# Optimization experiments

Hardware: AMD Instinct MI355X
Metric: run time of the kernel (lower is better)

Reference implementation:

```python
import jax, jax.numpy as jnp
import numpy as np

E, D, H, T = 64, 512, 1024, 256  # num_experts, dim, hidden_dim, tokens


def setup_inputs() -> dict:
    key = jax.random.key(0)
    k1, k2, k3, k4 = jax.random.split(key, 4)
    x = jax.random.normal(k1, (T, D), dtype=jnp.float32)
    expert_idx = jax.random.randint(k2, (T,), 0, E, dtype=jnp.int64)
    # kaiming_uniform-ish init scale for the batched expert weights
    fc1_w = jax.random.normal(k3, (E, H, D), dtype=jnp.float32) * 0.02  # [E, hidden, dim]
    fc2_w = jax.random.normal(k4, (E, D, H), dtype=jnp.float32) * 0.02  # [E, dim, hidden]
    return {"x": x, "expert_idx": expert_idx, "fc1_w": fc1_w, "fc2_w": fc2_w}


def reference(x, expert_idx, fc1_w, fc2_w):
    # Gather full expert weight matrices per token (faithful to torch module),
    # then per-token matvec: out = silu(x @ W1^T) @ W2^T
    w1 = fc1_w[expert_idx]                      # [T, H, D]
    w2 = fc2_w[expert_idx]                      # [T, D, H]
    h = jax.nn.silu(jnp.einsum('td,thd->th', x, w1))  # [T, H]
    out = jnp.einsum('th,tdh->td', h, w2)             # [T, D]
    return out
```

## Files before the change

### kernel.cpp

```cpp
#include <hip/hip_runtime.h>
#include <math.h>

#define NE 64
#define ND 512
#define NH 1024
#define NT 256
#define NC 8
#define NC2 4


__device__ __forceinline__ int build_group(const int* __restrict__ idx, int e,
                                           int* tok_lds, int* wsum) {
    const int t = threadIdx.x, wave = t >> 6, lane = t & 63;
    const bool m = (idx[t] == e);
    const unsigned long long mask = __ballot(m);
    if (lane == 0) wsum[wave] = __popcll(mask);
    __syncthreads();
    int before = 0;
#pragma unroll
    for (int w = 0; w < 3; ++w) before += (w < wave) ? wsum[w] : 0;
    const int nt = wsum[0] + wsum[1] + wsum[2] + wsum[3];
    if (m) {
        int pos = before + __popcll(mask & ((1ull << lane) - 1ull));
        tok_lds[pos] = t;
    }
    __syncthreads();
    if (nt > 0 && t >= nt && t < nt + NC) tok_lds[t] = tok_lds[0];
    __syncthreads();
    return nt;
}

__device__ __forceinline__ float fused_reduce8_64(float v[NC], int lane) {
#pragma unroll
    for (int i = 0; i < 4; ++i) {
        float lo = v[i], hi = v[i + 4];
        float send = (lane & 1) ? lo : hi;
        float recv = __shfl_xor(send, 1);
        v[i] = ((lane & 1) ? hi : lo) + recv;
    }
#pragma unroll
    for (int i = 0; i < 2; ++i) {
        float lo = v[i], hi = v[i + 2];
        float send = (lane & 2) ? lo : hi;
        float recv = __shfl_xor(send, 2);
        v[i] = ((lane & 2) ? hi : lo) + recv;
    }
    {
        float lo = v[0], hi = v[1];
        float send = (lane & 4) ? lo : hi;
        float recv = __shfl_xor(send, 4);
        v[0] = ((lane & 4) ? hi : lo) + recv;
    }
    v[0] += __shfl_xor(v[0], 8);
    v[0] += __shfl_xor(v[0], 16);
    v[0] += __shfl_xor(v[0], 32);
    return v[0];
}

__device__ __forceinline__ float fused_reduce4_64(float v[4], int lane) {
#pragma unroll
    for (int i = 0; i < 2; ++i) {
        float lo = v[i], hi = v[i + 2];
        float send = (lane & 1) ? lo : hi;
        float recv = __shfl_xor(send, 1);
        v[i] = ((lane & 1) ? hi : lo) + recv;
    }
    {
        float lo = v[0], hi = v[1];
        float send = (lane & 2) ? lo : hi;
        float recv = __shfl_xor(send, 2);
        v[0] = ((lane & 2) ? hi : lo) + recv;
    }
    v[0] += __shfl_xor(v[0], 4);
    v[0] += __shfl_xor(v[0], 8);
    v[0] += __shfl_xor(v[0], 16);
    v[0] += __shfl_xor(v[0], 32);
    return v[0];
}

__global__ __launch_bounds__(256) void fc1_kernel(
    const float* __restrict__ x, const float* __restrict__ w1,
    const int* __restrict__ idx, float* __restrict__ h) {
    __shared__ int tok_lds[NT + NC];
    __shared__ int wsum[4];
    __shared__ float xs[NC][ND];
    const int e  = blockIdx.x >> 5;
    const int ch = blockIdx.x & 31;
    const int tid = threadIdx.x, wave = tid >> 6, lane = tid & 63;
    const int nt = build_group(idx, e, tok_lds, wsum);
    if (nt == 0) return;
    const float* w1e = w1 + (size_t)e * NH * ND;
    const int jw = ch * 32 + wave * 8;

    for (int base = 0; base < nt; base += NC) {
        __syncthreads();
        for (int i = tid; i < NC * (ND / 4); i += 256) {
            int t = i >> 7, k = (i & 127) * 4;
            *(float4*)&xs[t][k] =
                *(const float4*)(x + (size_t)tok_lds[base + t] * ND + k);
        }
        __syncthreads();

#pragma unroll 4
        for (int r = 0; r < 8; ++r) {
            const float* wr = w1e + (size_t)(jw + r) * ND;
            const float4 wa = *(const float4*)(wr + lane * 4);
            const float4 wb = *(const float4*)(wr + 256 + lane * 4);
            float acc[NC];
#pragma unroll
            for (int t = 0; t < NC; ++t) {
                const float4 xa = *(const float4*)&xs[t][lane * 4];
                const float4 xb = *(const float4*)&xs[t][256 + lane * 4];
                acc[t] = wa.x * xa.x + wa.y * xa.y + wa.z * xa.z + wa.w * xa.w
                       + wb.x * xb.x + wb.y * xb.y + wb.z * xb.z + wb.w * xb.w;
            }
            float p = fused_reduce8_64(acc, lane);
            if (lane < NC) {
                int t = ((lane & 1) << 2) | (lane & 2) | ((lane >> 2) & 1);
                if (base + t < nt) {
                    int tk = tok_lds[base + t];
                    float s = p / (1.0f + __expf(-p));
                    h[(size_t)tk * NH + (jw + r)] = s;
                }
            }
        }
    }
}

__global__ __launch_bounds__(256) void fc2_kernel(
    const float* __restrict__ h, const float* __restrict__ w2,
    const int* __restrict__ idx, float* __restrict__ out) {
    __shared__ int tok_lds[NT + NC];
    __shared__ int wsum[4];
    __shared__ float hs[NC2][NH];
    const int e  = blockIdx.x >> 5;
    const int ch = blockIdx.x & 31;
    const int tid = threadIdx.x, wave = tid >> 6, lane = tid & 63;
    const int nt = build_group(idx, e, tok_lds, wsum);
    if (nt == 0) return;
    const float* w2e = w2 + (size_t)e * ND * NH;
    const int d0 = ch * 16 + wave * 4;

    for (int base = 0; base < nt; base += NC2) {
        __syncthreads();
        for (int i = tid; i < NC2 * (NH / 4); i += 256) {
            int t = i >> 8, k = (i & 255) * 4;
            *(float4*)&hs[t][k] =
                *(const float4*)(h + (size_t)tok_lds[base + t] * NH + k);
        }
        __syncthreads();

#pragma unroll
        for (int r = 0; r < 4; ++r) {
            const float* wr = w2e + (size_t)(d0 + r) * NH;
            const float4 w0 = *(const float4*)(wr + lane * 4);
            const float4 w1v = *(const float4*)(wr + 256 + lane * 4);
            const float4 w2v = *(const float4*)(wr + 512 + lane * 4);
            const float4 w3v = *(const float4*)(wr + 768 + lane * 4);
            float acc[NC2];
#pragma unroll
            for (int t = 0; t < NC2; ++t) {
                const float4 h0 = *(const float4*)&hs[t][lane * 4];
                const float4 h1 = *(const float4*)&hs[t][256 + lane * 4];
                const float4 h2 = *(const float4*)&hs[t][512 + lane * 4];
                const float4 h3 = *(const float4*)&hs[t][768 + lane * 4];
                acc[t] = w0.x * h0.x + w0.y * h0.y + w0.z * h0.z + w0.w * h0.w
                       + w1v.x * h1.x + w1v.y * h1.y + w1v.z * h1.z + w1v.w * h1.w
                       + w2v.x * h2.x + w2v.y * h2.y + w2v.z * h2.z + w2v.w * h2.w
                       + w3v.x * h3.x + w3v.y * h3.y + w3v.z * h3.z + w3v.w * h3.w;
            }
            float p = fused_reduce4_64(acc, lane);
            if (lane < NC2) {
                int t = ((lane & 1) << 1) | ((lane >> 1) & 1);
                int slot = base + t;
                if (slot < nt) {
                    int tk = tok_lds[slot];
                    out[(size_t)tk * ND + (d0 + r)] = p;
                }
            }
        }
    }
}

extern "C" void kernel_launch(void* const* d_in, const int* in_sizes, int n_in,
                              void* d_out, int out_size, void* d_ws, size_t ws_size,
                              hipStream_t stream) {
    const float* x    = (const float*)d_in[0];
    const int*   eidx = (const int*)d_in[1];
    const float* fc1w = (const float*)d_in[2];
    const float* fc2w = (const float*)d_in[3];
    float* out = (float*)d_out;
    float* h   = (float*)d_ws;

    fc1_kernel<<<NE * 32, 256, 0, stream>>>(x, fc1w, eidx, h);
    fc2_kernel<<<NE * 32, 256, 0, stream>>>(h, fc2w, eidx, out);
}
```

Before: 66.50 us.

## Split K across wave pairs and keep activations in registers instead of LDS

Both kernels drop the shared-memory staging of token activations. Each thread now loads its own slice of x/h straight into registers. Waves are paired into teams that split the reduction dimension in half, so each wave handles more output rows over a shorter K span. Partial sums are combined through a small LDS buffer before SiLU and the store, and launch bounds request higher occupancy. This removes the large LDS tiles and their staging barriers, at the cost of an extra cross-wave reduction with two syncs per token chunk and redundant activation loads per wave.

```diff
diff --git a/kernel.cpp b/kernel.cpp
--- a/kernel.cpp
+++ b/kernel.cpp
@@ -78,107 +78,109 @@
     return v[0];
 }
 
-__global__ __launch_bounds__(256) void fc1_kernel(
+__global__ __launch_bounds__(256, 8) void fc1_kernel(
     const float* __restrict__ x, const float* __restrict__ w1,
     const int* __restrict__ idx, float* __restrict__ h) {
     __shared__ int tok_lds[NT + NC];
     __shared__ int wsum[4];
-    __shared__ float xs[NC][ND];
+    __shared__ float part[2][2][16][NC];
     const int e  = blockIdx.x >> 5;
     const int ch = blockIdx.x & 31;
     const int tid = threadIdx.x, wave = tid >> 6, lane = tid & 63;
+    const int team = wave >> 1, half = wave & 1;
     const int nt = build_group(idx, e, tok_lds, wsum);
     if (nt == 0) return;
     const float* w1e = w1 + (size_t)e * NH * ND;
-    const int jw = ch * 32 + wave * 8;
+    const int jb = ch * 32 + team * 16;
+    const int kb = half * 256 + lane * 4;
 
     for (int base = 0; base < nt; base += NC) {
-        __syncthreads();
-        for (int i = tid; i < NC * (ND / 4); i += 256) {
-            int t = i >> 7, k = (i & 127) * 4;
-            *(float4*)&xs[t][k] =
-                *(const float4*)(x + (size_t)tok_lds[base + t] * ND + k);
-        }
-        __syncthreads();
+        float4 xs[NC];
+#pragma unroll
+        for (int t = 0; t < NC; ++t)
+            xs[t] = *(const float4*)(x + (size_t)tok_lds[base + t] * ND + kb);
 
 #pragma unroll 4
-        for (int r = 0; r < 8; ++r) {
-            const float* wr = w1e + (size_t)(jw + r) * ND;
-            const float4 wa = *(const float4*)(wr + lane * 4);
-            const float4 wb = *(const float4*)(wr + 256 + lane * 4);
+        for (int r = 0; r < 16; ++r) {
+            const float4 wv = *(const float4*)(w1e + (size_t)(jb + r) * ND + kb);
             float acc[NC];
 #pragma unroll
-            for (int t = 0; t < NC; ++t) {
-                const float4 xa = *(const float4*)&xs[t][lane * 4];
-                const float4 xb = *(const float4*)&xs[t][256 + lane * 4];
-                acc[t] = wa.x * xa.x + wa.y * xa.y + wa.z * xa.z + wa.w * xa.w
-                       + wb.x * xb.x + wb.y * xb.y + wb.z * xb.z + wb.w * xb.w;
-            }
+            for (int t = 0; t < NC; ++t)
+                acc[t] = wv.x * xs[t].x + wv.y * xs[t].y
+                       + wv.z * xs[t].z + wv.w * xs[t].w;
             float p = fused_reduce8_64(acc, lane);
             if (lane < NC) {
                 int t = ((lane & 1) << 2) | (lane & 2) | ((lane >> 2) & 1);
-                if (base + t < nt) {
-                    int tk = tok_lds[base + t];
-                    float s = p / (1.0f + __expf(-p));
-                    h[(size_t)tk * NH + (jw + r)] = s;
-                }
+                part[team][half][r][t] = p;
             }
         }
+        __syncthreads();
+        {
+            const int cteam = tid >> 7, ct = (tid >> 4) & 7, cr = tid & 15;
+            if (base + ct < nt) {
+                float s = part[cteam][0][cr][ct] + part[cteam][1][cr][ct];
+                s = s / (1.0f + __expf(-s));
+                int tk = tok_lds[base + ct];
+                h[(size_t)tk * NH + (ch * 32 + cteam * 16 + cr)] = s;
+            }
+        }
+        __syncthreads();
     }
 }
 
-__global__ __launch_bounds__(256) void fc2_kernel(
+__global__ __launch_bounds__(256, 8) void fc2_kernel(
     const float* __restrict__ h, const float* __restrict__ w2,
     const int* __restrict__ idx, float* __restrict__ out) {
     __shared__ int tok_lds[NT + NC];
     __shared__ int wsum[4];
-    __shared__ float hs[NC2][NH];
+    __shared__ float part2[2][2][8][NC2];
     const int e  = blockIdx.x >> 5;
     const int ch = blockIdx.x & 31;
     const int tid = threadIdx.x, wave = tid >> 6, lane = tid & 63;
+    const int team = wave >> 1, half = wave & 1;
     const int nt = build_group(idx, e, tok_lds, wsum);
     if (nt == 0) return;
     const float* w2e = w2 + (size_t)e * ND * NH;
-    const int d0 = ch * 16 + wave * 4;
+    const int db = ch * 16 + team * 8;
+    const int kb = half * 512 + lane * 4;
 
     for (int base = 0; base < nt; base += NC2) {
-        __syncthreads();
-        for (int i = tid; i < NC2 * (NH / 4); i += 256) {
-            int t = i >> 8, k = (i & 255) * 4;
-            *(float4*)&hs[t][k] =
-                *(const float4*)(h + (size_t)tok_lds[base + t] * NH + k);
+        float4 ha[NC2], hb[NC2];
+#pragma unroll
+        for (int t = 0; t < NC2; ++t) {
+            const float* hr = h + (size_t)tok_lds[base + t] * NH;
+            ha[t] = *(const float4*)(hr + kb);
+            hb[t] = *(const float4*)(hr + kb + 256);
         }
-        __syncthreads();
 
-#pragma unroll
-        for (int r = 0; r < 4; ++r) {
-            const float* wr = w2e + (size_t)(d0 + r) * NH;
-            const float4 w0 = *(const float4*)(wr + lane * 4);
-            const float4 w1v = *(const float4*)(wr + 256 + lane * 4);
-            const float4 w2v = *(const float4*)(wr + 512 + lane * 4);
-            const float4 w3v = *(const float4*)(wr + 768 + lane * 4);
+#pragma unroll 4
+        for (int r = 0; r < 8; ++r) {
+            const float* wr = w2e + (size_t)(db + r) * NH;
+            const float4 wa = *(const float4*)(wr + kb);
+            const float4 wb = *(const float4*)(wr + kb + 256);
             float acc[NC2];
 #pragma unroll
-            for (int t = 0; t < NC2; ++t) {
-                const float4 h0 = *(const float4*)&hs[t][lane * 4];
-                const float4 h1 = *(const float4*)&hs[t][256 + lane * 4];
-                const float4 h2 = *(const float4*)&hs[t][512 + lane * 4];
-                const float4 h3 = *(const float4*)&hs[t][768 + lane * 4];
-                acc[t] = w0.x * h0.x + w0.y * h0.y + w0.z * h0.z + w0.w * h0.w
-                       + w1v.x * h1.x + w1v.y * h1.y + w1v.z * h1.z + w1v.w * h1.w
-                       + w2v.x * h2.x + w2v.y * h2.y + w2v.z * h2.z + w2v.w * h2.w
-                       + w3v.x * h3.x + w3v.y * h3.y + w3v.z * h3.z + w3v.w * h3.w;
-            }
+            for (int t = 0; t < NC2; ++t)
+                acc[t] = wa.x * ha[t].x + wa.y * ha[t].y
+                       + wa.z * ha[t].z + wa.w * ha[t].w
+                       + wb.x * hb[t].x + wb.y * hb[t].y
+                       + wb.z * hb[t].z + wb.w * hb[t].w;
             float p = fused_reduce4_64(acc, lane);
             if (lane < NC2) {
                 int t = ((lane & 1) << 1) | ((lane >> 1) & 1);
-                int slot = base + t;
-                if (slot < nt) {
-                    int tk = tok_lds[slot];
-                    out[(size_t)tk * ND + (d0 + r)] = p;
-                }
+                part2[team][half][r][t] = p;
             }
         }
+        __syncthreads();
+        if (tid < 64) {
+            const int cteam = tid >> 5, ct = (tid >> 3) & 3, cr = tid & 7;
+            if (base + ct < nt) {
+                float s = part2[cteam][0][cr][ct] + part2[cteam][1][cr][ct];
+                int tk = tok_lds[base + ct];
+                out[(size_t)tk * ND + (ch * 16 + cteam * 8 + cr)] = s;
+            }
+        }
+        __syncthreads();
     }
 }
 
```

Result: slower. 72.20 us (+8.6%).
